# Optimization experiments

Measured on AMD Instinct MI355X. Metric: run time of the kernel, lower is better.

Reference implementation:

```python
import jax, jax.numpy as jnp
import numpy as np

EPS = 1e-8  # torch.nn.CosineSimilarity default eps


def setup_inputs() -> dict:
    key = jax.random.key(0)
    ks = jax.random.split(key, 6)
    B, N, SD, HD, AD = 512, 256, 1024, 512, 256
    return {
        "state_emb": jax.random.normal(ks[0], (B, SD), dtype=jnp.float32),
        "hints_emb": jax.random.normal(ks[1], (B, N, HD), dtype=jnp.float32),
        "Ws": jax.random.normal(ks[2], (AD, SD), dtype=jnp.float32) * 0.02,
        "bs": jax.random.normal(ks[3], (AD,), dtype=jnp.float32) * 0.02,
        "Wh": jax.random.normal(ks[4], (AD, HD), dtype=jnp.float32) * 0.02,
        "bh": jax.random.normal(ks[5], (AD,), dtype=jnp.float32) * 0.02,
    }


def reference(state_emb, hints_emb, Ws, bs, Wh, bh):
    # Projections
    sp = state_emb @ Ws.T + bs                       # (B, A)
    hp = jnp.einsum("bnh,ah->bna", hints_emb, Wh) + bh  # (B, N, A)
    # Cosine similarity along feature dim (torch CosineSimilarity semantics)
    sn = jnp.maximum(jnp.linalg.norm(sp, axis=-1, keepdims=True), EPS)    # (B,1)
    hn = jnp.maximum(jnp.linalg.norm(hp, axis=-1), EPS)                   # (B,N)
    scores = jnp.einsum("ba,bna->bn", sp, hp) / (sn * hn)                 # (B,N)
    attn_weights = jax.nn.softmax(scores, axis=1)                         # (B,N)
    # Weighted sum over hints (original, unprojected embeddings)
    output = jnp.einsum("bn,bnh->bh", attn_weights, hints_emb)            # (B,HD)
    return output
```

## Files before the change

### kernel.cpp

```cpp
#include <hip/hip_runtime.h>
#include <hip/hip_bf16.h>

typedef __attribute__((ext_vector_type(8))) short bf16x8;
typedef __attribute__((ext_vector_type(4))) float f32x4;
typedef __attribute__((ext_vector_type(4))) unsigned int u32x4;

#define B_  512
#define N_  256
#define SD_ 1024
#define HD_ 512
#define AD_ 256

__device__ __forceinline__ unsigned short f2bf(float f) {
    unsigned int u = __float_as_uint(f);
    unsigned int r = (u + 0x7FFFu + ((u >> 16) & 1u)) >> 16;
    return (unsigned short)r;
}

__device__ __forceinline__ unsigned int cvtpk(float lo, float hi) {
    unsigned int r;
    asm("v_cvt_pk_bf16_f32 %0, %1, %2" : "=v"(r) : "v"(lo), "v"(hi));
    return r;
}

__device__ __forceinline__ void gload16(const float* g, char* l) {
    __builtin_amdgcn_global_load_lds(
        (const __attribute__((address_space(1))) unsigned int*)g,
        (__attribute__((address_space(3))) unsigned int*)l, 16, 0, 0);
}

__global__ void k0_pack(const float* __restrict__ Wh, unsigned short* __restrict__ whp) {
    int g = blockIdx.x * 256 + threadIdx.x;
    int ct  = g >> 10;
    int rem = g & 1023;
    int ks  = rem >> 6;
    int l   = rem & 63;
    int a   = ct * 16 + (l & 15);
    int kb  = ks * 32 + (l >> 4) * 8;
    const float* src = Wh + (size_t)a * HD_ + kb;
    float4 v0 = *(const float4*)(src);
    float4 v1 = *(const float4*)(src + 4);
    bf16x8 o;
    o[0] = (short)f2bf(v0.x); o[1] = (short)f2bf(v0.y);
    o[2] = (short)f2bf(v0.z); o[3] = (short)f2bf(v0.w);
    o[4] = (short)f2bf(v1.x); o[5] = (short)f2bf(v1.y);
    o[6] = (short)f2bf(v1.z); o[7] = (short)f2bf(v1.w);
    ((bf16x8*)whp)[g] = o;
}

__global__ __launch_bounds__(512) void k1_proj(
    const float* __restrict__ state, const float* __restrict__ Ws,
    const float* __restrict__ bs,
    float* __restrict__ sn, float* __restrict__ spv)
{
    __shared__ float st[2][SD_];
    __shared__ float spl[2][AD_];
    __shared__ float red[2][AD_];
    int tid = threadIdx.x, lane = tid & 63, w = tid >> 6;
    int b0 = blockIdx.x * 2;
    ((float4*)st)[tid] = ((const float4*)(state + (size_t)b0 * SD_))[tid];
    __syncthreads();
    float4 s0[4], s1[4];
    #pragma unroll
    for (int seg = 0; seg < 4; ++seg) {
        s0[seg] = *(const float4*)&st[0][seg * 256 + lane * 4];
        s1[seg] = *(const float4*)&st[1][seg * 256 + lane * 4];
    }
    #pragma unroll 2
    for (int i = 0; i < 32; ++i) {
        int a = w * 32 + i;
        const float4* wr = (const float4*)(Ws + (size_t)a * SD_);
        float p0 = 0.f, p1 = 0.f;
        #pragma unroll
        for (int seg = 0; seg < 4; ++seg) {
            float4 wv = wr[seg * 64 + lane];
            p0 += wv.x * s0[seg].x + wv.y * s0[seg].y + wv.z * s0[seg].z + wv.w * s0[seg].w;
            p1 += wv.x * s1[seg].x + wv.y * s1[seg].y + wv.z * s1[seg].z + wv.w * s1[seg].w;
        }
        #pragma unroll
        for (int d = 1; d < 64; d <<= 1) { p0 += __shfl_xor(p0, d); p1 += __shfl_xor(p1, d); }
        if (lane == 0) {
            float bsa = bs[a];
            spl[0][a] = p0 + bsa;
            spl[1][a] = p1 + bsa;
        }
    }
    __syncthreads();
    int tb = tid >> 8, t = tid & 255;
    float sv = spl[tb][t];
    spv[(size_t)(b0 + tb) * AD_ + t] = sv;
    red[tb][t] = sv * sv;
    __syncthreads();
    for (int s = 128; s > 0; s >>= 1) { if (t < s) red[tb][t] += red[tb][t + s]; __syncthreads(); }
    if (t == 0) sn[b0 + tb] = fmaxf(sqrtf(red[tb][0]), 1e-8f);
}

__global__ __launch_bounds__(512, 2) void k2_scores(
    const float* __restrict__ hints, const unsigned short* __restrict__ whp,
    const float* __restrict__ spv, const float* __restrict__ sn,
    const float* __restrict__ bh, float* __restrict__ scores)
{
    __shared__ __align__(16) char smem[69632];
    char* bufA = smem;
    char* bufB = smem + 32768;
    float* sp_lds  = (float*)(smem + 65536);
    float* bh_lds  = (float*)(smem + 66560);
    float* norm2p  = (float*)(smem + 67584);
    float* nump    = (float*)(smem + 68608);

    int tid = threadIdx.x, lane = tid & 63, w = tid >> 6;
    int b = blockIdx.x;
    const float* hb = hints + (size_t)b * N_ * HD_;
    if (tid < 64) ((float4*)sp_lds)[tid] = ((const float4*)(spv + (size_t)b * AD_))[tid];
    else if (tid < 128) ((float4*)bh_lds)[tid - 64] = ((const float4*)bh)[tid - 64];
    float snb = sn[b];
    int cl = lane & 15, q = lane >> 4;
    int rh = (w & 1) * 32;
    int g  = w >> 1;
    int srow = tid >> 5;
    int sgp  = (tid & 31) >> 1;
    int shalf = tid & 1;
    __syncthreads();
    float bhv[4], spc[4];
    #pragma unroll
    for (int ci = 0; ci < 4; ++ci) {
        int col = (g * 4 + ci) * 16 + cl;
        bhv[ci] = bh_lds[col];
        spc[ci] = sp_lds[col];
    }

#define STAGE(c, buf) do {                                                     \
    int mcs = (c) >> 2, kcs = (c) & 3;                                         \
    _Pragma("unroll")                                                          \
    for (int s = 0; s < 4; ++s) {                                              \
        int row = s * 16 + srow;                                               \
        const float* gsrc = hb + (size_t)(mcs * 64 + row) * HD_ + kcs * 128    \
                            + ((sgp ^ (row & 15)) << 3) + shalf * 4;           \
        gload16(gsrc, (buf) + s * 8192 + tid * 16);                            \
    }                                                                          \
} while (0)

    STAGE(0, bufA);
    __syncthreads();

    for (int mc = 0; mc < 4; ++mc) {
        f32x4 acc[2][4];
        #pragma unroll
        for (int mf = 0; mf < 2; ++mf)
            #pragma unroll
            for (int ci = 0; ci < 4; ++ci) acc[mf][ci] = (f32x4){0.f, 0.f, 0.f, 0.f};

        #pragma unroll
        for (int kc = 0; kc < 4; ++kc) {
            int c = mc * 4 + kc;
            if (c + 1 < 16) STAGE(c + 1, (c & 1) ? bufA : bufB);
            const char* bR = (c & 1) ? bufB : bufA;
            #pragma unroll
            for (int kk = 0; kk < 4; ++kk) {
                bf16x8 bfr[4];
                #pragma unroll
                for (int ci = 0; ci < 4; ++ci)
                    bfr[ci] = ((const bf16x8*)whp)[((g * 4 + ci) * 16 + kc * 4 + kk) * 64 + lane];
                #pragma unroll
                for (int mf = 0; mf < 2; ++mf) {
                    int r = rh + mf * 16 + cl;
                    const char* ap = bR + r * 512 + (((kk * 4 + q) ^ cl) << 5);
                    float4 lo = *(const float4*)ap;
                    float4 hi = *(const float4*)(ap + 16);
                    u32x4 t;
                    t[0] = cvtpk(lo.x, lo.y);
                    t[1] = cvtpk(lo.z, lo.w);
                    t[2] = cvtpk(hi.x, hi.y);
                    t[3] = cvtpk(hi.z, hi.w);
                    bf16x8 afr = __builtin_bit_cast(bf16x8, t);
                    #pragma unroll
                    for (int ci = 0; ci < 4; ++ci)
                        acc[mf][ci] = __builtin_amdgcn_mfma_f32_16x16x32_bf16(afr, bfr[ci], acc[mf][ci], 0, 0, 0);
                }
            }
            __syncthreads();
        }

        #pragma unroll
        for (int mf = 0; mf < 2; ++mf) {
            #pragma unroll
            for (int r = 0; r < 4; ++r) {
                float vv = 0.f, uu = 0.f;
                #pragma unroll
                for (int ci = 0; ci < 4; ++ci) {
                    float h = acc[mf][ci][r] + bhv[ci];
                    vv += h * h;
                    uu += spc[ci] * h;
                }
                vv += __shfl_xor(vv, 1); uu += __shfl_xor(uu, 1);
                vv += __shfl_xor(vv, 2); uu += __shfl_xor(uu, 2);
                vv += __shfl_xor(vv, 4); uu += __shfl_xor(uu, 4);
                vv += __shfl_xor(vv, 8); uu += __shfl_xor(uu, 8);
                if (cl == 0) {
                    int row = rh + mf * 16 + q * 4 + r;
                    norm2p[g * 64 + row] = vv;
                    nump[g * 64 + row]   = uu;
                }
            }
        }
        __syncthreads();
        if (tid < 64) {
            float n2 = norm2p[tid] + norm2p[64 + tid] + norm2p[128 + tid] + norm2p[192 + tid];
            float nm = nump[tid] + nump[64 + tid] + nump[128 + tid] + nump[192 + tid];
            float hn = fmaxf(sqrtf(n2), 1e-8f);
            scores[(size_t)b * N_ + mc * 64 + tid] = nm / (snb * hn);
        }
        __syncthreads();
    }
#undef STAGE
}

__global__ __launch_bounds__(512) void k2b_out(
    const float* __restrict__ hints, const float* __restrict__ scores,
    float* __restrict__ out)
{
    __shared__ float sc[N_];
    __shared__ float red[N_];
    __shared__ float wsm[N_];
    __shared__ float scratch[2048];
    int tid = threadIdx.x;
    int b = blockIdx.x;
    const float* hb = hints + (size_t)b * N_ * HD_;
    if (tid < 256) sc[tid] = scores[(size_t)b * N_ + tid];
    __syncthreads();
    if (tid < 256) red[tid] = sc[tid];
    __syncthreads();
    for (int s = 128; s > 0; s >>= 1) { if (tid < s) red[tid] = fmaxf(red[tid], red[tid + s]); __syncthreads(); }
    float mx = red[0];
    __syncthreads();
    if (tid < 256) { float e = __expf(sc[tid] - mx); sc[tid] = e; red[tid] = e; }
    __syncthreads();
    for (int s = 128; s > 0; s >>= 1) { if (tid < s) red[tid] += red[tid + s]; __syncthreads(); }
    float inv = 1.f / red[0];
    __syncthreads();
    if (tid < 256) wsm[tid] = sc[tid] * inv;
    __syncthreads();

    int hg = tid & 127, ng = tid >> 7;
    const float* hbe = hb + (size_t)(ng * 64) * HD_ + hg * 4;
    float ax = 0.f, ay = 0.f, az = 0.f, aw = 0.f;
    #pragma unroll 8
    for (int n = 0; n < 64; ++n) {
        float4 hv = *(const float4*)(hbe + (size_t)n * HD_);
        float wn = wsm[ng * 64 + n];
        ax += wn * hv.x; ay += wn * hv.y; az += wn * hv.z; aw += wn * hv.w;
    }
    *(float4*)(scratch + ng * 512 + hg * 4) = (float4){ax, ay, az, aw};
    __syncthreads();
    out[(size_t)b * HD_ + tid] =
        scratch[tid] + scratch[512 + tid] + scratch[1024 + tid] + scratch[1536 + tid];
}

extern "C" void kernel_launch(void* const* d_in, const int* in_sizes, int n_in,
                              void* d_out, int out_size, void* d_ws, size_t ws_size,
                              hipStream_t stream) {
    const float* state = (const float*)d_in[0];
    const float* hints = (const float*)d_in[1];
    const float* Ws    = (const float*)d_in[2];
    const float* bs    = (const float*)d_in[3];
    const float* Wh    = (const float*)d_in[4];
    const float* bh    = (const float*)d_in[5];
    float* out = (float*)d_out;

    float* sn = (float*)d_ws;
    float* spv = sn + B_;
    unsigned short* whp = (unsigned short*)(spv + (size_t)B_ * AD_);
    float* scores = (float*)(whp + (size_t)AD_ * HD_);

    k0_pack<<<64, 256, 0, stream>>>(Wh, whp);
    k1_proj<<<B_ / 2, 512, 0, stream>>>(state, Ws, bs, sn, spv);
    k2_scores<<<B_, 512, 0, stream>>>(hints, whp, spv, sn, bh, scores);
    k2b_out<<<B_, 512, 0, stream>>>(hints, scores, out);
}
```

Before: 172.0 us.

## Restructure score kernel into 256-thread blocks over 32-row slices with triple buffering

```diff
diff --git a/kernel.cpp b/kernel.cpp
--- a/kernel.cpp
+++ b/kernel.cpp
@@ -95,55 +95,55 @@
     if (t == 0) sn[b0 + tb] = fmaxf(sqrtf(red[tb][0]), 1e-8f);
 }
 
-__global__ __launch_bounds__(512, 2) void k2_scores(
+__global__ __launch_bounds__(256, 2) void k2_scores(
     const float* __restrict__ hints, const unsigned short* __restrict__ whp,
     const float* __restrict__ spv, const float* __restrict__ sn,
     const float* __restrict__ bh, float* __restrict__ scores)
 {
-    __shared__ __align__(16) char smem[69632];
-    char* bufA = smem;
-    char* bufB = smem + 32768;
-    float* sp_lds  = (float*)(smem + 65536);
-    float* bh_lds  = (float*)(smem + 66560);
-    float* norm2p  = (float*)(smem + 67584);
-    float* nump    = (float*)(smem + 68608);
+    __shared__ __align__(16) char smem[59968];
+    char* bufs = smem;
+    float* bh_lds  = (float*)(smem + 49152);
+    float* spv_lds = (float*)(smem + 50176);
+    float* sn_lds  = (float*)(smem + 58368);
+    float* norm2p  = (float*)(smem + 58432);
+    float* nump    = (float*)(smem + 58944);
 
     int tid = threadIdx.x, lane = tid & 63, w = tid >> 6;
     int b = blockIdx.x;
-    const float* hb = hints + (size_t)b * N_ * HD_;
-    if (tid < 64) ((float4*)sp_lds)[tid] = ((const float4*)(spv + (size_t)b * AD_))[tid];
-    else if (tid < 128) ((float4*)bh_lds)[tid - 64] = ((const float4*)bh)[tid - 64];
-    float snb = sn[b];
     int cl = lane & 15, q = lane >> 4;
-    int rh = (w & 1) * 32;
-    int g  = w >> 1;
-    int srow = tid >> 5;
-    int sgp  = (tid & 31) >> 1;
-    int shalf = tid & 1;
-    __syncthreads();
-    float bhv[4], spc[4];
-    #pragma unroll
-    for (int ci = 0; ci < 4; ++ci) {
-        int col = (g * 4 + ci) * 16 + cl;
-        bhv[ci] = bh_lds[col];
-        spc[ci] = sp_lds[col];
-    }
-
-#define STAGE(c, buf) do {                                                     \
-    int mcs = (c) >> 2, kcs = (c) & 3;                                         \
+    int brow = b >> 3;
+
+#define STAGE(c) do {                                                          \
+    int gg = ((c) >> 2) * 512 + b;                                             \
+    const float* gb = hints + (size_t)gg * (32 * 512) + ((c) & 3) * 128;       \
+    char* bp = bufs + ((c) % 3) * 16384;                                       \
     _Pragma("unroll")                                                          \
-    for (int s = 0; s < 4; ++s) {                                              \
-        int row = s * 16 + srow;                                               \
-        const float* gsrc = hb + (size_t)(mcs * 64 + row) * HD_ + kcs * 128    \
-                            + ((sgp ^ (row & 15)) << 3) + shalf * 4;           \
-        gload16(gsrc, (buf) + s * 8192 + tid * 16);                            \
+    for (int j = 0; j < 4; ++j) {                                              \
+        int e = j * 256 + tid;                                                 \
+        int row = e >> 5, pg = e & 31;                                         \
+        gload16(gb + (size_t)row * 512 + ((pg ^ row) << 2), bp + e * 16);      \
     }                                                                          \
 } while (0)
 
-    STAGE(0, bufA);
-    __syncthreads();
-
-    for (int mc = 0; mc < 4; ++mc) {
+    STAGE(0);
+    STAGE(1);
+    if (tid < 64) ((float4*)bh_lds)[tid] = ((const float4*)bh)[tid];
+    #pragma unroll
+    for (int i = 0; i < 8; ++i)
+        spv_lds[i * 256 + tid] = spv[(size_t)(i * 64 + brow) * 256 + tid];
+    if (tid < 8) sn_lds[tid] = sn[tid * 64 + brow];
+    __syncthreads();
+
+    float bhv[4];
+    #pragma unroll
+    for (int ci = 0; ci < 4; ++ci) bhv[ci] = bh_lds[(w * 4 + ci) * 16 + cl];
+
+    for (int i = 0; i < 8; ++i) {
+        float snb = sn_lds[i];
+        float spc[4];
+        #pragma unroll
+        for (int ci = 0; ci < 4; ++ci)
+            spc[ci] = spv_lds[i * 256 + (w * 4 + ci) * 16 + cl];
         f32x4 acc[2][4];
         #pragma unroll
         for (int mf = 0; mf < 2; ++mf)
@@ -152,21 +152,24 @@
 
         #pragma unroll
         for (int kc = 0; kc < 4; ++kc) {
-            int c = mc * 4 + kc;
-            if (c + 1 < 16) STAGE(c + 1, (c & 1) ? bufA : bufB);
-            const char* bR = (c & 1) ? bufB : bufA;
-            #pragma unroll
-            for (int kk = 0; kk < 4; ++kk) {
-                bf16x8 bfr[4];
+            int c = i * 4 + kc;
+            bf16x8 bfr[16];
+            #pragma unroll
+            for (int k4 = 0; k4 < 4; ++k4)
                 #pragma unroll
                 for (int ci = 0; ci < 4; ++ci)
-                    bfr[ci] = ((const bf16x8*)whp)[((g * 4 + ci) * 16 + kc * 4 + kk) * 64 + lane];
+                    bfr[k4 * 4 + ci] = ((const bf16x8*)whp)
+                        [((w * 4 + ci) * 16 + kc * 4 + k4) * 64 + lane];
+            if (c + 2 < 32) STAGE(c + 2);
+            const char* bp = bufs + (c % 3) * 16384;
+            #pragma unroll
+            for (int k4 = 0; k4 < 4; ++k4) {
                 #pragma unroll
                 for (int mf = 0; mf < 2; ++mf) {
-                    int r = rh + mf * 16 + cl;
-                    const char* ap = bR + r * 512 + (((kk * 4 + q) ^ cl) << 5);
-                    float4 lo = *(const float4*)ap;
-                    float4 hi = *(const float4*)(ap + 16);
+                    int r = mf * 16 + cl;
+                    int lg = k4 * 8 + q * 2;
+                    float4 lo = *(const float4*)(bp + r * 512 + ((lg ^ r) << 4));
+                    float4 hi = *(const float4*)(bp + r * 512 + (((lg + 1) ^ r) << 4));
                     u32x4 t;
                     t[0] = cvtpk(lo.x, lo.y);
                     t[1] = cvtpk(lo.z, lo.w);
@@ -175,20 +178,22 @@
                     bf16x8 afr = __builtin_bit_cast(bf16x8, t);
                     #pragma unroll
                     for (int ci = 0; ci < 4; ++ci)
-                        acc[mf][ci] = __builtin_amdgcn_mfma_f32_16x16x32_bf16(afr, bfr[ci], acc[mf][ci], 0, 0, 0);
+                        acc[mf][ci] = __builtin_amdgcn_mfma_f32_16x16x32_bf16(
+                            afr, bfr[k4 * 4 + ci], acc[mf][ci], 0, 0, 0);
                 }
             }
-            __syncthreads();
+            asm volatile("s_waitcnt lgkmcnt(0)" ::: "memory");
+            __builtin_amdgcn_s_barrier();
         }
 
         #pragma unroll
         for (int mf = 0; mf < 2; ++mf) {
             #pragma unroll
-            for (int r = 0; r < 4; ++r) {
+            for (int rr = 0; rr < 4; ++rr) {
                 float vv = 0.f, uu = 0.f;
                 #pragma unroll
                 for (int ci = 0; ci < 4; ++ci) {
-                    float h = acc[mf][ci][r] + bhv[ci];
+                    float h = acc[mf][ci][rr] + bhv[ci];
                     vv += h * h;
                     uu += spc[ci] * h;
                 }
@@ -197,20 +202,22 @@
                 vv += __shfl_xor(vv, 4); uu += __shfl_xor(uu, 4);
                 vv += __shfl_xor(vv, 8); uu += __shfl_xor(uu, 8);
                 if (cl == 0) {
-                    int row = rh + mf * 16 + q * 4 + r;
-                    norm2p[g * 64 + row] = vv;
-                    nump[g * 64 + row]   = uu;
+                    int idx = w * 32 + mf * 16 + q * 4 + rr;
+                    norm2p[idx] = vv;
+                    nump[idx]   = uu;
                 }
             }
         }
-        __syncthreads();
-        if (tid < 64) {
-            float n2 = norm2p[tid] + norm2p[64 + tid] + norm2p[128 + tid] + norm2p[192 + tid];
-            float nm = nump[tid] + nump[64 + tid] + nump[128 + tid] + nump[192 + tid];
+        asm volatile("s_waitcnt lgkmcnt(0)" ::: "memory");
+        __builtin_amdgcn_s_barrier();
+        if (tid < 32) {
+            float n2 = norm2p[tid] + norm2p[32 + tid] + norm2p[64 + tid] + norm2p[96 + tid];
+            float nm = nump[tid] + nump[32 + tid] + nump[64 + tid] + nump[96 + tid];
             float hn = fmaxf(sqrtf(n2), 1e-8f);
-            scores[(size_t)b * N_ + mc * 64 + tid] = nm / (snb * hn);
-        }
-        __syncthreads();
+            scores[(size_t)(i * 512 + b) * 32 + tid] = nm / (snb * hn);
+        }
+        asm volatile("s_waitcnt lgkmcnt(0)" ::: "memory");
+        __builtin_amdgcn_s_barrier();
     }
 #undef STAGE
 }
@@ -274,6 +281,6 @@
 
     k0_pack<<<64, 256, 0, stream>>>(Wh, whp);
     k1_proj<<<B_ / 2, 512, 0, stream>>>(state, Ws, bs, sn, spv);
-    k2_scores<<<B_, 512, 0, stream>>>(hints, whp, spv, sn, bh, scores);
+    k2_scores<<<B_, 256, 0, stream>>>(hints, whp, spv, sn, bh, scores);
     k2b_out<<<B_, 512, 0, stream>>>(hints, scores, out);
 }
```

Result: slower. 253.5 us (+47.4%).
